# Performance work log

Measured on AMD Instinct MI355X. Metric: run time of the kernel, lower is better.

## Reference

```python
import jax, jax.numpy as jnp
import numpy as np

B, T, I, H, A = 32, 1024, 64, 512, 16


def setup_inputs() -> dict:
    key = jax.random.key(0)
    ks = jax.random.split(key, 8)
    # xavier-normal-ish scales (faithful to init distribution family, values are arbitrary for a numeric baseline)
    def xavier(k, shape):
        fan_in, fan_out = shape[0], shape[1]
        std = (2.0 / (fan_in + fan_out)) ** 0.5
        return jax.random.normal(k, shape, dtype=jnp.float32) * std
    inp = jax.random.normal(ks[0], (B, T, I), dtype=jnp.float32)
    hn = jax.random.normal(ks[1], (1, B, H), dtype=jnp.float32)
    w_hh = xavier(ks[2], (H, H))          # weight_l0_hh: [hid, hid]
    w_ih = xavier(ks[3], (I, H))          # weight_l0_ih: [inp, hid]
    # torch Linear(hid, hid): y = x @ W.T + b; store already-transposed [in, out]
    fc1_w = xavier(ks[4], (H, H))
    fc1_b = jax.random.normal(ks[5], (H,), dtype=jnp.float32) * 0.01
    fc2_w = xavier(ks[6], (H, A))
    fc2_b = jax.random.normal(ks[7], (A,), dtype=jnp.float32) * 0.01
    return {"inp": inp, "hn": hn, "w_hh": w_hh, "w_ih": w_ih,
            "fc1_w": fc1_w, "fc1_b": fc1_b, "fc2_w": fc2_w, "fc2_b": fc2_b}


def reference(inp, hn, w_hh, w_ih, fc1_w, fc1_b, fc2_w, fc2_b):
    h0 = hn[0]                                  # [B, H]  (hn.squeeze(0))
    # precompute input projection for all steps: [T, B, H]
    x_proj = jnp.einsum('bti,ih->tbh', inp, w_ih)
    def step(h, xp_t):
        h_next = jax.nn.sigmoid(h @ w_hh + xp_t)  # [B, H]
        return h_next, h_next
    _, hs = jax.lax.scan(step, h0, x_proj)       # hs: [T, B, H]
    rnn_out = jnp.swapaxes(hs, 0, 1)             # [B, T, H]
    hn_last = rnn_out[:, -1, :][None]            # [1, B, H]
    hidden = jax.nn.relu(rnn_out @ fc1_w + fc1_b)
    out = jax.nn.sigmoid(hidden @ fc2_w + fc2_b) # [B, T, A]
    return (out, hn_last, rnn_out)
```

## Files before the change

### kernel.cpp

```cpp
#include <hip/hip_runtime.h>
#include <hip/hip_bf16.h>

#define Bz 32
#define Tz 1024
#define Iz 64
#define Hz 512
#define Az 16

#define OFF_HN  (Bz*Tz*Az)
#define OFF_RNN (OFF_HN + Bz*Hz)

typedef unsigned short u16;
typedef unsigned int u32;
typedef unsigned long long u64;
typedef __attribute__((ext_vector_type(8))) unsigned short u16x8;
typedef __attribute__((ext_vector_type(8))) __bf16 bf16x8;
typedef __attribute__((ext_vector_type(4))) float f32x4;

#define WS_WIH  0x00000u
#define WS_WHT  0x10000u
#define WS_W1T  0x90000u

__device__ __forceinline__ u16 f2bf(float f) {
  union { float f; unsigned int i; } x; x.f = f;
  unsigned int r = (x.i + 0x7FFFu + ((x.i >> 16) & 1u)) >> 16;
  return (u16)r;
}
__device__ __forceinline__ float bf2f(u16 u) {
  union { unsigned int i; float f; } x; x.i = ((unsigned int)u) << 16; return x.f;
}
__device__ __forceinline__ float sigmoidf_(float z) {
  return 1.0f / (1.0f + __expf(-z));
}

__global__ void prep_kernel(const float* __restrict__ whh,
                            const float* __restrict__ wih,
                            const float* __restrict__ w1,
                            u16* __restrict__ whhT,
                            u16* __restrict__ wih_bf,
                            u16* __restrict__ w1t_bf) {
  int idx = blockIdx.x * 256 + threadIdx.x;
  if (idx < 262144) {
    int n = idx >> 9, k = idx & 511;
    whhT[idx] = f2bf(whh[k * Hz + n]);
  } else if (idx < 294912) {
    int i = idx - 262144;
    wih_bf[i] = f2bf(wih[i]);
  } else if (idx < 557056) {
    int j = idx - 294912;
    int n = j >> 9, k = j & 511;
    w1t_bf[n * Hz + k] = f2bf(w1[k * Hz + n]);
  }
}

__global__ __launch_bounds__(256, 2) void xproj_kernel(
    const float* __restrict__ inp,
    const u16* __restrict__ wih_bf,
    float* __restrict__ xp)
{
  __shared__ u16 wl[512][72];

  const int tid  = threadIdx.x;
  const int lane = tid & 63;
  const int wv   = tid >> 6;
  const int ln   = lane & 15;
  const int q    = lane >> 4;

#pragma unroll
  for (int i = 0; i < Iz; ++i) {
    wl[tid][i]       = wih_bf[i * Hz + tid];
    wl[tid + 256][i] = wih_bf[i * Hz + tid + 256];
  }
  __syncthreads();

  const size_t row0 = (size_t)blockIdx.x * 64 + wv * 16;
  const float* ip = inp + (row0 + ln) * Iz + q * 8;
  f32x4 x0 = *(const f32x4*)(ip);
  f32x4 x1 = *(const f32x4*)(ip + 4);
  f32x4 x2 = *(const f32x4*)(ip + 32);
  f32x4 x3 = *(const f32x4*)(ip + 36);
  u16x8 ax0, ax1;
#pragma unroll
  for (int j = 0; j < 4; ++j) {
    ax0[j]     = f2bf(x0[j]);
    ax0[4 + j] = f2bf(x1[j]);
    ax1[j]     = f2bf(x2[j]);
    ax1[4 + j] = f2bf(x3[j]);
  }

  for (int nt = 0; nt < 32; ++nt) {
    bf16x8 b0 = __builtin_bit_cast(bf16x8, *(const u16x8*)&wl[nt * 16 + ln][q * 8]);
    bf16x8 b1 = __builtin_bit_cast(bf16x8, *(const u16x8*)&wl[nt * 16 + ln][32 + q * 8]);
    f32x4 a = {0.f, 0.f, 0.f, 0.f};
    a = __builtin_amdgcn_mfma_f32_16x16x32_bf16(
        __builtin_bit_cast(bf16x8, ax0), b0, a, 0, 0, 0);
    a = __builtin_amdgcn_mfma_f32_16x16x32_bf16(
        __builtin_bit_cast(bf16x8, ax1), b1, a, 0, 0, 0);
#pragma unroll
    for (int r = 0; r < 4; ++r)
      xp[(row0 + q * 4 + r) * Hz + nt * 16 + ln] = a[r];
  }
}

__global__ __launch_bounds__(512, 2) void rnn_scan_kernel(
    const float* __restrict__ hn,
    const u16* __restrict__ whhT,
    float* __restrict__ out_rnn,
    float* __restrict__ out_hn)
{
  __shared__ u16 wlds[512][136];
  __shared__ u16 hlds[16][528];

  const int tid  = threadIdx.x;
  const int lane = tid & 63;
  const int w    = tid >> 6;
  const int ln   = lane & 15;
  const int q    = lane >> 4;
  const int r0   = blockIdx.x * 16;
  const int c0   = w * 64;

  bf16x8 bhh[4][12];
#pragma unroll
  for (int ct = 0; ct < 4; ++ct)
#pragma unroll
    for (int ks = 0; ks < 12; ++ks)
      bhh[ct][ks] = __builtin_bit_cast(
          bf16x8, *(const u16x8*)(whhT + (size_t)(c0 + ct * 16 + ln) * Hz +
                                  ks * 32 + q * 8));

#pragma unroll
  for (int j = 0; j < 16; ++j)
    *(u16x8*)&wlds[tid][j * 8] =
        *(const u16x8*)(whhT + (size_t)tid * Hz + 384 + j * 8);

  {
    const int row = tid >> 5, c = (tid & 31) * 16;
    const float* hp = hn + (size_t)(r0 + row) * Hz + c;
    f32x4 a0 = *(const f32x4*)(hp);
    f32x4 a1 = *(const f32x4*)(hp + 4);
    f32x4 a2 = *(const f32x4*)(hp + 8);
    f32x4 a3 = *(const f32x4*)(hp + 12);
    u16x8 p0, p1;
#pragma unroll
    for (int j = 0; j < 4; ++j) {
      p0[j] = f2bf(a0[j]); p0[4 + j] = f2bf(a1[j]);
      p1[j] = f2bf(a2[j]); p1[4 + j] = f2bf(a3[j]);
    }
    *(u16x8*)&hlds[row][c]     = p0;
    *(u16x8*)&hlds[row][c + 8] = p1;
  }
  __syncthreads();

  for (int t = 0; t < Tz; ++t) {
    float xp[4][4];
#pragma unroll
    for (int r = 0; r < 4; ++r) {
      const float* xrow =
          out_rnn + ((size_t)(r0 + q * 4 + r) * Tz + t) * Hz + c0 + ln;
#pragma unroll
      for (int ct = 0; ct < 4; ++ct) xp[ct][r] = xrow[ct * 16];
    }

    f32x4 acc[4];
#pragma unroll
    for (int ct = 0; ct < 4; ++ct) acc[ct] = (f32x4){0.f, 0.f, 0.f, 0.f};

#pragma unroll
    for (int ks = 0; ks < 12; ++ks) {
      bf16x8 A = __builtin_bit_cast(
          bf16x8, *(const u16x8*)&hlds[ln][ks * 32 + q * 8]);
#pragma unroll
      for (int ct = 0; ct < 4; ++ct)
        acc[ct] = __builtin_amdgcn_mfma_f32_16x16x32_bf16(
            A, bhh[ct][ks], acc[ct], 0, 0, 0);
    }
#pragma unroll
    for (int lk = 0; lk < 4; ++lk) {
      bf16x8 A = __builtin_bit_cast(
          bf16x8, *(const u16x8*)&hlds[ln][(12 + lk) * 32 + q * 8]);
#pragma unroll
      for (int ct = 0; ct < 4; ++ct) {
        bf16x8 Bf = __builtin_bit_cast(
            bf16x8, *(const u16x8*)&wlds[c0 + ct * 16 + ln][lk * 32 + q * 8]);
        acc[ct] = __builtin_amdgcn_mfma_f32_16x16x32_bf16(
            A, Bf, acc[ct], 0, 0, 0);
      }
    }

    float hv[4][4];
#pragma unroll
    for (int ct = 0; ct < 4; ++ct)
#pragma unroll
      for (int r = 0; r < 4; ++r) hv[ct][r] = sigmoidf_(acc[ct][r] + xp[ct][r]);

    __syncthreads();

#pragma unroll
    for (int ct = 0; ct < 4; ++ct)
#pragma unroll
      for (int r = 0; r < 4; ++r) {
        u32 mine  = (u32)f2bf(hv[ct][r]);
        u32 other = (u32)__shfl_xor((int)mine, 1, 64);
        if (!(ln & 1))
          *(u32*)&hlds[q * 4 + r][c0 + ct * 16 + ln] = mine | (other << 16);
      }
    __syncthreads();

#pragma unroll
    for (int r = 0; r < 4; ++r) {
      float* orow =
          out_rnn + ((size_t)(r0 + q * 4 + r) * Tz + t) * Hz + c0 + ln;
#pragma unroll
      for (int ct = 0; ct < 4; ++ct) orow[ct * 16] = hv[ct][r];
    }
    if (t == Tz - 1) {
#pragma unroll
      for (int r = 0; r < 4; ++r)
#pragma unroll
        for (int ct = 0; ct < 4; ++ct)
          out_hn[(size_t)(r0 + q * 4 + r) * Hz + c0 + ct * 16 + ln] = hv[ct][r];
    }
  }
}

__global__ __launch_bounds__(256, 2) void fc_kernel(
    const float* __restrict__ X,
    const u16* __restrict__ w1t,
    const float* __restrict__ b1,
    const float* __restrict__ w2,
    const float* __restrict__ b2,
    float* __restrict__ out)
{
  __shared__ u16 smem[18432];
  u16* As = smem;
  u16* Bs = smem + 9216;
  u16* Ht = smem;

  const int tid  = threadIdx.x;
  const int lane = tid & 63;
  const int wv   = tid >> 6;
  const int ln   = lane & 15, q = lane >> 4;
  const int mq   = (wv & 1) * 64, nq = (wv >> 1) * 64;
  const size_t r0 = (size_t)blockIdx.x * 128;
  const int om = tid >> 1;
  const int oa = (tid & 1) * 8;

  float oacc[8];
#pragma unroll
  for (int j = 0; j < 8; ++j) oacc[j] = 0.f;

  for (int nt = 0; nt < 4; ++nt) {
    const int n0 = nt * 128;
    f32x4 acc[4][4];
#pragma unroll
    for (int mi = 0; mi < 4; ++mi)
#pragma unroll
      for (int ni = 0; ni < 4; ++ni) acc[mi][ni] = (f32x4){0.f, 0.f, 0.f, 0.f};

    for (int kb = 0; kb < 8; ++kb) {
      const int K0 = kb * 64;
      __syncthreads();
      for (int i = tid; i < 1024; i += 256) {
        int row = i >> 3, c = (i & 7) * 8;
        f32x4 lo = *(const f32x4*)(X + (r0 + row) * Hz + K0 + c);
        f32x4 hi = *(const f32x4*)(X + (r0 + row) * Hz + K0 + c + 4);
        u16x8 pxx;
#pragma unroll
        for (int j = 0; j < 4; ++j) { pxx[j] = f2bf(lo[j]); pxx[4 + j] = f2bf(hi[j]); }
        *(u16x8*)(As + row * 72 + c) = pxx;
      }
      for (int i = tid; i < 1024; i += 256) {
        int row = i >> 3, c = (i & 7) * 8;
        *(u16x8*)(Bs + row * 72 + c) =
            *(const u16x8*)(w1t + (size_t)(n0 + row) * Hz + K0 + c);
      }
      __syncthreads();
#pragma unroll
      for (int kt = 0; kt < 2; ++kt) {
        bf16x8 af[4], bfr[4];
#pragma unroll
        for (int mi = 0; mi < 4; ++mi)
          af[mi] = __builtin_bit_cast(
              bf16x8,
              *(const u16x8*)(As + (mq + mi * 16 + ln) * 72 + kt * 32 + q * 8));
#pragma unroll
        for (int ni = 0; ni < 4; ++ni)
          bfr[ni] = __builtin_bit_cast(
              bf16x8,
              *(const u16x8*)(Bs + (nq + ni * 16 + ln) * 72 + kt * 32 + q * 8));
#pragma unroll
        for (int mi = 0; mi < 4; ++mi)
#pragma unroll
          for (int ni = 0; ni < 4; ++ni)
            acc[mi][ni] = __builtin_amdgcn_mfma_f32_16x16x32_bf16(
                af[mi], bfr[ni], acc[mi][ni], 0, 0, 0);
      }
    }
    __syncthreads();

#pragma unroll
    for (int ni = 0; ni < 4; ++ni) {
      float bb = b1[n0 + nq + ni * 16 + ln];
#pragma unroll
      for (int mi = 0; mi < 4; ++mi)
#pragma unroll
        for (int r = 0; r < 4; ++r) {
          float h = fmaxf(acc[mi][ni][r] + bb, 0.f);
          Ht[(mq + mi * 16 + q * 4 + r) * 136 + nq + ni * 16 + ln] = f2bf(h);
        }
    }
    __syncthreads();

    for (int n = 0; n < 128; ++n) {
      float hv = bf2f(Ht[om * 136 + n]);
      const float* w2p = w2 + (size_t)(n0 + n) * Az + oa;
#pragma unroll
      for (int j = 0; j < 8; ++j) oacc[j] += hv * w2p[j];
    }
  }

#pragma unroll
  for (int j = 0; j < 8; ++j)
    out[(r0 + om) * Az + oa + j] = sigmoidf_(oacc[j] + b2[oa + j]);
}

extern "C" void kernel_launch(void* const* d_in, const int* in_sizes, int n_in,
                              void* d_out, int out_size, void* d_ws, size_t ws_size,
                              hipStream_t stream) {
  int idx_inp = 0, idx_hn = 1, idx_wih = 3, idx_b1 = 5, idx_w2 = 6, idx_b2 = 7;
  int amb1 = -1, amb2 = -1, found = 0;
  for (int i = 0; i < 8 && i < n_in; ++i) {
    switch (in_sizes[i]) {
      case 2097152: idx_inp = i; found |= 1; break;
      case 16384:   idx_hn  = i; found |= 2; break;
      case 32768:   idx_wih = i; found |= 4; break;
      case 512:     idx_b1  = i; found |= 8; break;
      case 8192:    idx_w2  = i; found |= 16; break;
      case 16:      idx_b2  = i; found |= 32; break;
      case 262144:  if (amb1 < 0) amb1 = i; else amb2 = i; break;
    }
  }
  int idx_whh = 2, idx_w1 = 4;
  if (amb1 >= 0 && amb2 >= 0 && found == 63) {
    if (idx_b1 < idx_inp) { idx_w1 = amb1; idx_whh = amb2; }
    else                  { idx_whh = amb1; idx_w1 = amb2; }
  }

  const float* inp = (const float*)d_in[idx_inp];
  const float* hn  = (const float*)d_in[idx_hn];
  const float* whh = (const float*)d_in[idx_whh];
  const float* wih = (const float*)d_in[idx_wih];
  const float* w1  = (const float*)d_in[idx_w1];
  const float* b1  = (const float*)d_in[idx_b1];
  const float* w2  = (const float*)d_in[idx_w2];
  const float* b2  = (const float*)d_in[idx_b2];

  float* out     = (float*)d_out;
  float* out_hn  = out + OFF_HN;
  float* out_rnn = out + OFF_RNN;

  char* ws    = (char*)d_ws;
  u16* wih_bf = (u16*)(ws + WS_WIH);
  u16* whhT   = (u16*)(ws + WS_WHT);
  u16* w1t_bf = (u16*)(ws + WS_W1T);

  prep_kernel<<<dim3(2176), dim3(256), 0, stream>>>(whh, wih, w1,
                                                    whhT, wih_bf, w1t_bf);
  xproj_kernel<<<dim3(512), dim3(256), 0, stream>>>(inp, wih_bf, out_rnn);
  rnn_scan_kernel<<<dim3(2), dim3(512), 0, stream>>>(
      hn, whhT, out_rnn, out_hn);
  fc_kernel<<<dim3(256), dim3(256), 0, stream>>>(
      out_rnn, w1t_bf, b1, w2, b2, out);
}
```

Before: 3.725 ms.

## Stream part of W_hh from global each step instead of holding in registers

Shrinks the register-resident slice of W_hh from 12 to 8 k-slices. The remaining 4 slices are reloaded from global memory/L2 every timestep in two staged batches, and empty asm barriers keep those loads from being hoisted out of the loop or reordered. Launch bounds drop to one block per SIMD-pair, which allows more registers per thread. The goal is to relieve register pressure and spilling, at the cost of extra per-step global loads on the serial recurrence path.

Measured after the change: 6.211 ms. 1.67x slower.

```diff
diff --git a/kernel.cpp b/kernel.cpp
--- a/kernel.cpp
+++ b/kernel.cpp
@@ -102,7 +102,7 @@
   }
 }
 
-__global__ __launch_bounds__(512, 2) void rnn_scan_kernel(
+__global__ __launch_bounds__(512, 1) void rnn_scan_kernel(
     const float* __restrict__ hn,
     const u16* __restrict__ whhT,
     float* __restrict__ out_rnn,
@@ -119,14 +119,19 @@
   const int r0   = blockIdx.x * 16;
   const int c0   = w * 64;
 
-  bf16x8 bhh[4][12];
+  bf16x8 bhh[4][8];
 #pragma unroll
   for (int ct = 0; ct < 4; ++ct)
 #pragma unroll
-    for (int ks = 0; ks < 12; ++ks)
+    for (int ks = 0; ks < 8; ++ks)
       bhh[ct][ks] = __builtin_bit_cast(
           bf16x8, *(const u16x8*)(whhT + (size_t)(c0 + ct * 16 + ln) * Hz +
                                   ks * 32 + q * 8));
+
+  u64 wb0 = (u64)(whhT + (size_t)(c0 + 0 * 16 + ln) * Hz + 256 + q * 8);
+  u64 wb1 = (u64)(whhT + (size_t)(c0 + 1 * 16 + ln) * Hz + 256 + q * 8);
+  u64 wb2 = (u64)(whhT + (size_t)(c0 + 2 * 16 + ln) * Hz + 256 + q * 8);
+  u64 wb3 = (u64)(whhT + (size_t)(c0 + 3 * 16 + ln) * Hz + 256 + q * 8);
 
 #pragma unroll
   for (int j = 0; j < 16; ++j)
@@ -152,6 +157,15 @@
   __syncthreads();
 
   for (int t = 0; t < Tz; ++t) {
+    u64 a0 = wb0, a1 = wb1, a2 = wb2, a3 = wb3;
+    asm volatile("" : "+v"(a0), "+v"(a1), "+v"(a2), "+v"(a3));
+
+    u16x8 s1[4][2];
+    s1[0][0] = *(const u16x8*)(a0);  s1[0][1] = *(const u16x8*)((const u16*)a0 + 32);
+    s1[1][0] = *(const u16x8*)(a1);  s1[1][1] = *(const u16x8*)((const u16*)a1 + 32);
+    s1[2][0] = *(const u16x8*)(a2);  s1[2][1] = *(const u16x8*)((const u16*)a2 + 32);
+    s1[3][0] = *(const u16x8*)(a3);  s1[3][1] = *(const u16x8*)((const u16*)a3 + 32);
+
     float xp[4][4];
 #pragma unroll
     for (int r = 0; r < 4; ++r) {
@@ -166,7 +180,7 @@
     for (int ct = 0; ct < 4; ++ct) acc[ct] = (f32x4){0.f, 0.f, 0.f, 0.f};
 
 #pragma unroll
-    for (int ks = 0; ks < 12; ++ks) {
+    for (int ks = 0; ks < 8; ++ks) {
       bf16x8 A = __builtin_bit_cast(
           bf16x8, *(const u16x8*)&hlds[ln][ks * 32 + q * 8]);
 #pragma unroll
@@ -174,6 +188,29 @@
         acc[ct] = __builtin_amdgcn_mfma_f32_16x16x32_bf16(
             A, bhh[ct][ks], acc[ct], 0, 0, 0);
     }
+
+#pragma unroll
+    for (int s = 0; s < 2; ++s) {
+      bf16x8 A = __builtin_bit_cast(
+          bf16x8, *(const u16x8*)&hlds[ln][(8 + s) * 32 + q * 8]);
+      acc[0] = __builtin_amdgcn_mfma_f32_16x16x32_bf16(
+          A, __builtin_bit_cast(bf16x8, s1[0][s]), acc[0], 0, 0, 0);
+      acc[1] = __builtin_amdgcn_mfma_f32_16x16x32_bf16(
+          A, __builtin_bit_cast(bf16x8, s1[1][s]), acc[1], 0, 0, 0);
+      acc[2] = __builtin_amdgcn_mfma_f32_16x16x32_bf16(
+          A, __builtin_bit_cast(bf16x8, s1[2][s]), acc[2], 0, 0, 0);
+      acc[3] = __builtin_amdgcn_mfma_f32_16x16x32_bf16(
+          A, __builtin_bit_cast(bf16x8, s1[3][s]), acc[3], 0, 0, 0);
+    }
+
+    asm volatile("" : "+v"(a0), "+v"(a1), "+v"(a2), "+v"(a3) : "v"(acc[0]));
+
+    u16x8 s2[4][2];
+    s2[0][0] = *(const u16x8*)((const u16*)a0 + 64);  s2[0][1] = *(const u16x8*)((const u16*)a0 + 96);
+    s2[1][0] = *(const u16x8*)((const u16*)a1 + 64);  s2[1][1] = *(const u16x8*)((const u16*)a1 + 96);
+    s2[2][0] = *(const u16x8*)((const u16*)a2 + 64);  s2[2][1] = *(const u16x8*)((const u16*)a2 + 96);
+    s2[3][0] = *(const u16x8*)((const u16*)a3 + 64);  s2[3][1] = *(const u16x8*)((const u16*)a3 + 96);
+
 #pragma unroll
     for (int lk = 0; lk < 4; ++lk) {
       bf16x8 A = __builtin_bit_cast(
@@ -185,6 +222,20 @@
         acc[ct] = __builtin_amdgcn_mfma_f32_16x16x32_bf16(
             A, Bf, acc[ct], 0, 0, 0);
       }
+    }
+
+#pragma unroll
+    for (int s = 0; s < 2; ++s) {
+      bf16x8 A = __builtin_bit_cast(
+          bf16x8, *(const u16x8*)&hlds[ln][(10 + s) * 32 + q * 8]);
+      acc[0] = __builtin_amdgcn_mfma_f32_16x16x32_bf16(
+          A, __builtin_bit_cast(bf16x8, s2[0][s]), acc[0], 0, 0, 0);
+      acc[1] = __builtin_amdgcn_mfma_f32_16x16x32_bf16(
+          A, __builtin_bit_cast(bf16x8, s2[1][s]), acc[1], 0, 0, 0);
+      acc[2] = __builtin_amdgcn_mfma_f32_16x16x32_bf16(
+          A, __builtin_bit_cast(bf16x8, s2[2][s]), acc[2], 0, 0, 0);
+      acc[3] = __builtin_amdgcn_mfma_f32_16x16x32_bf16(
+          A, __builtin_bit_cast(bf16x8, s2[3][s]), acc[3], 0, 0, 0);
     }
 
     float hv[4][4];
```

## Split RNN scan hidden dimension across block pairs with global flag sync

Applied to the files above, without the earlier changes.

The recurrent scan moves from 2 workgroups, each owning 16 batch rows and all 512 hidden columns, to pairs of workgroups that each own half the hidden columns. Each block keeps its entire W_hh slice in registers, which removes the shared-memory weight tile. Per step, a block computes its local half of the matmul, spins on a global flag for its partner's half, reads that half from a 4-slot global ring buffer, and then finishes. The aim is to halve per-step MFMA work per block and raise register residency, at the cost of cross-block spin-wait latency on every step. The flags use relaxed atomics only, and 16 blocks are launched where 12 exit immediately, presumably to spread the active blocks across XCDs/CUs.

After: 9.520 ms. 156% more time.

```diff
diff --git a/kernel.cpp b/kernel.cpp
--- a/kernel.cpp
+++ b/kernel.cpp
@@ -6,6 +6,7 @@
 #define Iz 64
 #define Hz 512
 #define Az 16
+#define NF 4
 
 #define OFF_HN  (Bz*Tz*Az)
 #define OFF_RNN (OFF_HN + Bz*Hz)
@@ -17,9 +18,12 @@
 typedef __attribute__((ext_vector_type(8))) __bf16 bf16x8;
 typedef __attribute__((ext_vector_type(4))) float f32x4;
 
-#define WS_WIH  0x00000u
-#define WS_WHT  0x10000u
-#define WS_W1T  0x90000u
+#define WS_FLAGS 0x00000u
+#define WS_RING  0x21000u
+#define WS_WHT   0x41000u
+#define WS_WIH   0xC1000u
+#define WS_W1T   0xD1000u
+#define WS_ZERO  0x05000u
 
 __device__ __forceinline__ u16 f2bf(float f) {
   union { float f; unsigned int i; } x; x.f = f;
@@ -102,124 +106,153 @@
   }
 }
 
-__global__ __launch_bounds__(512, 2) void rnn_scan_kernel(
+__global__ __launch_bounds__(512, 1) void rnn_scan_kernel(
     const float* __restrict__ hn,
     const u16* __restrict__ whhT,
     float* __restrict__ out_rnn,
-    float* __restrict__ out_hn)
+    float* __restrict__ out_hn,
+    int* __restrict__ flags,
+    u16* __restrict__ hbuf)
 {
-  __shared__ u16 wlds[512][136];
-  __shared__ u16 hlds[16][528];
+  __shared__ u16 hl[16][256];
+  __shared__ u16 pl[16][256];
 
   const int tid  = threadIdx.x;
   const int lane = tid & 63;
   const int w    = tid >> 6;
   const int ln   = lane & 15;
   const int q    = lane >> 4;
-  const int r0   = blockIdx.x * 16;
-  const int c0   = w * 64;
-
-  bf16x8 bhh[4][12];
-#pragma unroll
-  for (int ct = 0; ct < 4; ++ct)
-#pragma unroll
-    for (int ks = 0; ks < 12; ++ks)
+  const int bid  = blockIdx.x;
+  if ((bid & 7) >= 2) return;
+  const int p     = bid & 7;
+  const int qh    = bid >> 3;
+  const int r0    = p * 16;
+  const int cbase = qh * 256;
+  const int obase = 256 - cbase;
+  const int c0    = cbase + w * 32;
+  const int fid      = p * 2 + qh;
+  const int fpartner = p * 2 + (1 - qh);
+
+  bf16x8 bhh[2][16];
+#pragma unroll
+  for (int ct = 0; ct < 2; ++ct)
+#pragma unroll
+    for (int ks = 0; ks < 16; ++ks)
       bhh[ct][ks] = __builtin_bit_cast(
           bf16x8, *(const u16x8*)(whhT + (size_t)(c0 + ct * 16 + ln) * Hz +
                                   ks * 32 + q * 8));
 
-#pragma unroll
-  for (int j = 0; j < 16; ++j)
-    *(u16x8*)&wlds[tid][j * 8] =
-        *(const u16x8*)(whhT + (size_t)tid * Hz + 384 + j * 8);
-
   {
-    const int row = tid >> 5, c = (tid & 31) * 16;
-    const float* hp = hn + (size_t)(r0 + row) * Hz + c;
-    f32x4 a0 = *(const f32x4*)(hp);
-    f32x4 a1 = *(const f32x4*)(hp + 4);
-    f32x4 a2 = *(const f32x4*)(hp + 8);
-    f32x4 a3 = *(const f32x4*)(hp + 12);
-    u16x8 p0, p1;
-#pragma unroll
-    for (int j = 0; j < 4; ++j) {
-      p0[j] = f2bf(a0[j]); p0[4 + j] = f2bf(a1[j]);
-      p1[j] = f2bf(a2[j]); p1[4 + j] = f2bf(a3[j]);
-    }
-    *(u16x8*)&hlds[row][c]     = p0;
-    *(u16x8*)&hlds[row][c + 8] = p1;
+    const int row = tid >> 5;
+    const int ch  = tid & 31;
+    const float* hp = hn + (size_t)(r0 + row) * Hz + cbase + ch * 8;
+    f32x4 a = *(const f32x4*)(hp);
+    f32x4 b = *(const f32x4*)(hp + 4);
+    u16x8 px;
+#pragma unroll
+    for (int j = 0; j < 4; ++j) { px[j] = f2bf(a[j]); px[4 + j] = f2bf(b[j]); }
+    *(u16x8*)&hl[row][(ch ^ (row & 7)) * 8] = px;
+    u64 two[2] = {0, 0};
+    *(u16x8*)two = px;
+    u64* rp = (u64*)(hbuf) + ((size_t)(r0 + row) * Hz + cbase + ch * 8) / 4;
+    __hip_atomic_store(rp,     two[0], __ATOMIC_RELAXED, __HIP_MEMORY_SCOPE_AGENT);
+    __hip_atomic_store(rp + 1, two[1], __ATOMIC_RELAXED, __HIP_MEMORY_SCOPE_AGENT);
   }
   __syncthreads();
+  if (tid == 0)
+    __hip_atomic_store(&flags[fid], 1, __ATOMIC_RELAXED,
+                       __HIP_MEMORY_SCOPE_AGENT);
 
   for (int t = 0; t < Tz; ++t) {
-    float xp[4][4];
+    float xp[2][4];
 #pragma unroll
     for (int r = 0; r < 4; ++r) {
       const float* xrow =
           out_rnn + ((size_t)(r0 + q * 4 + r) * Tz + t) * Hz + c0 + ln;
-#pragma unroll
-      for (int ct = 0; ct < 4; ++ct) xp[ct][r] = xrow[ct * 16];
-    }
-
-    f32x4 acc[4];
-#pragma unroll
-    for (int ct = 0; ct < 4; ++ct) acc[ct] = (f32x4){0.f, 0.f, 0.f, 0.f};
-
-#pragma unroll
-    for (int ks = 0; ks < 12; ++ks) {
+      xp[0][r] = xrow[0];
+      xp[1][r] = xrow[16];
+    }
+
+    f32x4 acc[2];
+    acc[0] = (f32x4){0.f, 0.f, 0.f, 0.f};
+    acc[1] = (f32x4){0.f, 0.f, 0.f, 0.f};
+
+#pragma unroll
+    for (int ks = 0; ks < 8; ++ks) {
       bf16x8 A = __builtin_bit_cast(
-          bf16x8, *(const u16x8*)&hlds[ln][ks * 32 + q * 8]);
-#pragma unroll
-      for (int ct = 0; ct < 4; ++ct)
-        acc[ct] = __builtin_amdgcn_mfma_f32_16x16x32_bf16(
-            A, bhh[ct][ks], acc[ct], 0, 0, 0);
-    }
-#pragma unroll
-    for (int lk = 0; lk < 4; ++lk) {
+          bf16x8, *(const u16x8*)&hl[ln][((ks * 4 + q) ^ (ln & 7)) * 8]);
+      acc[0] = __builtin_amdgcn_mfma_f32_16x16x32_bf16(
+          A, bhh[0][qh * 8 + ks], acc[0], 0, 0, 0);
+      acc[1] = __builtin_amdgcn_mfma_f32_16x16x32_bf16(
+          A, bhh[1][qh * 8 + ks], acc[1], 0, 0, 0);
+    }
+
+    {
+      int got;
+      do {
+        got = __hip_atomic_load(&flags[t * NF + fpartner], __ATOMIC_RELAXED,
+                                __HIP_MEMORY_SCOPE_AGENT);
+      } while (!got);
+    }
+
+    {
+      const int row = tid >> 5;
+      const int ch  = tid & 31;
+      const u64* src = (const u64*)(hbuf + (size_t)(t & 3) * (Bz * Hz)) +
+                       ((size_t)(r0 + row) * Hz + obase + ch * 8) / 4;
+      u64 v0 = __hip_atomic_load(src,     __ATOMIC_RELAXED,
+                                 __HIP_MEMORY_SCOPE_AGENT);
+      u64 v1 = __hip_atomic_load(src + 1, __ATOMIC_RELAXED,
+                                 __HIP_MEMORY_SCOPE_AGENT);
+      u64* dst = (u64*)&pl[row][(ch ^ (row & 7)) * 8];
+      dst[0] = v0;
+      dst[1] = v1;
+    }
+    __syncthreads();
+
+#pragma unroll
+    for (int ks = 0; ks < 8; ++ks) {
       bf16x8 A = __builtin_bit_cast(
-          bf16x8, *(const u16x8*)&hlds[ln][(12 + lk) * 32 + q * 8]);
-#pragma unroll
-      for (int ct = 0; ct < 4; ++ct) {
-        bf16x8 Bf = __builtin_bit_cast(
-            bf16x8, *(const u16x8*)&wlds[c0 + ct * 16 + ln][lk * 32 + q * 8]);
-        acc[ct] = __builtin_amdgcn_mfma_f32_16x16x32_bf16(
-            A, Bf, acc[ct], 0, 0, 0);
-      }
-    }
-
-    float hv[4][4];
-#pragma unroll
-    for (int ct = 0; ct < 4; ++ct)
-#pragma unroll
-      for (int r = 0; r < 4; ++r) hv[ct][r] = sigmoidf_(acc[ct][r] + xp[ct][r]);
-
-    __syncthreads();
-
-#pragma unroll
-    for (int ct = 0; ct < 4; ++ct)
+          bf16x8, *(const u16x8*)&pl[ln][((ks * 4 + q) ^ (ln & 7)) * 8]);
+      acc[0] = __builtin_amdgcn_mfma_f32_16x16x32_bf16(
+          A, bhh[0][(1 - qh) * 8 + ks], acc[0], 0, 0, 0);
+      acc[1] = __builtin_amdgcn_mfma_f32_16x16x32_bf16(
+          A, bhh[1][(1 - qh) * 8 + ks], acc[1], 0, 0, 0);
+    }
+
+    float hv[2][4];
+    u16* ring_next = hbuf + (size_t)((t + 1) & 3) * (Bz * Hz);
+#pragma unroll
+    for (int ct = 0; ct < 2; ++ct)
 #pragma unroll
       for (int r = 0; r < 4; ++r) {
+        hv[ct][r] = sigmoidf_(acc[ct][r] + xp[ct][r]);
         u32 mine  = (u32)f2bf(hv[ct][r]);
         u32 other = (u32)__shfl_xor((int)mine, 1, 64);
-        if (!(ln & 1))
-          *(u32*)&hlds[q * 4 + r][c0 + ct * 16 + ln] = mine | (other << 16);
+        if (!(ln & 1)) {
+          u32 pk = mine | (other << 16);
+          const int row_l = q * 4 + r;
+          const int col_l = w * 32 + ct * 16 + ln;
+          __hip_atomic_store(
+              (u32*)(ring_next + (size_t)(r0 + row_l) * Hz + cbase + col_l),
+              pk, __ATOMIC_RELAXED, __HIP_MEMORY_SCOPE_AGENT);
+          *(u32*)&hl[row_l][((col_l >> 3) ^ (row_l & 7)) * 8 + (col_l & 7)] = pk;
+        }
       }
     __syncthreads();
-
-#pragma unroll
-    for (int r = 0; r < 4; ++r) {
-      float* orow =
-          out_rnn + ((size_t)(r0 + q * 4 + r) * Tz + t) * Hz + c0 + ln;
-#pragma unroll
-      for (int ct = 0; ct < 4; ++ct) orow[ct * 16] = hv[ct][r];
-    }
-    if (t == Tz - 1) {
-#pragma unroll
-      for (int r = 0; r < 4; ++r)
-#pragma unroll
-        for (int ct = 0; ct < 4; ++ct)
-          out_hn[(size_t)(r0 + q * 4 + r) * Hz + c0 + ct * 16 + ln] = hv[ct][r];
-    }
+    if (tid == 0)
+      __hip_atomic_store(&flags[(t + 1) * NF + fid], 1, __ATOMIC_RELAXED,
+                         __HIP_MEMORY_SCOPE_AGENT);
+
+#pragma unroll
+    for (int ct = 0; ct < 2; ++ct)
+#pragma unroll
+      for (int r = 0; r < 4; ++r) {
+        const int grow = r0 + q * 4 + r;
+        const int gcol = c0 + ct * 16 + ln;
+        out_rnn[((size_t)grow * Tz + t) * Hz + gcol] = hv[ct][r];
+        if (t == Tz - 1) out_hn[(size_t)grow * Hz + gcol] = hv[ct][r];
+      }
   }
 }
 
@@ -360,15 +393,18 @@
   float* out_rnn = out + OFF_RNN;
 
   char* ws    = (char*)d_ws;
+  int* flags  = (int*)(ws + WS_FLAGS);
+  u16* hbuf   = (u16*)(ws + WS_RING);
+  u16* whhT   = (u16*)(ws + WS_WHT);
   u16* wih_bf = (u16*)(ws + WS_WIH);
-  u16* whhT   = (u16*)(ws + WS_WHT);
   u16* w1t_bf = (u16*)(ws + WS_W1T);
 
+  (void)hipMemsetAsync(d_ws, 0, WS_ZERO, stream);
   prep_kernel<<<dim3(2176), dim3(256), 0, stream>>>(whh, wih, w1,
                                                     whhT, wih_bf, w1t_bf);
   xproj_kernel<<<dim3(512), dim3(256), 0, stream>>>(inp, wih_bf, out_rnn);
-  rnn_scan_kernel<<<dim3(2), dim3(512), 0, stream>>>(
-      hn, whhT, out_rnn, out_hn);
+  rnn_scan_kernel<<<dim3(16), dim3(512), 0, stream>>>(
+      hn, whhT, out_rnn, out_hn, flags, hbuf);
   fc_kernel<<<dim3(256), dim3(256), 0, stream>>>(
       out_rnn, w1t_bf, b1, w2, b2, out);
 }
```
